# Kernel optimization log

Hardware: AMD Instinct MI355X
Metric: run time of the kernel (lower is better)

## Reference

```python
import jax, jax.numpy as jnp
import numpy as np

DIM_HEAD = 128
HEADS = 16
SCALE = DIM_HEAD ** -0.5


def rotate_half(t):
    # '... (j d) -> ... j d' with j=2: split into first/second halves
    x1, x2 = jnp.split(t, 2, axis=-1)
    return jnp.concatenate((-x2, x1), axis=-1)


def apply_rope(pos, t):
    # pos: [n, d]; t: [..., n, d]
    return t * jnp.cos(pos) + rotate_half(t) * jnp.sin(pos)


def setup_inputs() -> dict:
    key = jax.random.key(0)
    k0, k1, k2, k3 = jax.random.split(key, 4)
    b, n, dim = 2, 2048, 2048
    inner = HEADS * DIM_HEAD
    return {
        "x": jax.random.normal(k0, (b, n, dim), jnp.float32),
        "Wq": jax.random.normal(k1, (dim, inner), jnp.float32) * 0.02,
        "Wkv": jax.random.normal(k2, (dim, 2 * DIM_HEAD), jnp.float32) * 0.02,
        "Wout": jax.random.normal(k3, (inner, dim), jnp.float32) * 0.02,
    }


def reference(x, Wq, Wkv, Wout):
    b, n, dim = x.shape
    # projections from the UN-normalized x (norm in original is dead code)
    q = x @ Wq                               # [b, n, h*d]
    kv = x @ Wkv                             # [b, n, 2d]
    k, v = jnp.split(kv, 2, axis=-1)         # each [b, n, d] (multi-query)
    q = q.reshape(b, n, HEADS, DIM_HEAD).transpose(0, 2, 1, 3)  # [b,h,n,d]

    # rotary positions
    inv_freq = 1.0 / (10000.0 ** (jnp.arange(0, DIM_HEAD, 2, dtype=jnp.float32) / DIM_HEAD))
    freqs = jnp.arange(n, dtype=jnp.float32)[:, None] * inv_freq[None, :]
    pos = jnp.concatenate((freqs, freqs), axis=-1)  # [n, d]

    q = apply_rope(pos, q) * SCALE
    k = apply_rope(pos, k)

    sim = jnp.einsum('bhid,bjd->bhij', q, k)  # [b,h,n,n]
    causal_mask = jnp.triu(jnp.ones((n, n), dtype=bool), 1)
    neg = -jnp.finfo(sim.dtype).max
    sim = jnp.where(causal_mask, neg, sim)
    sim = sim - jax.lax.stop_gradient(jnp.max(sim, axis=-1, keepdims=True))
    attn = jax.nn.softmax(sim, axis=-1)

    out = jnp.einsum('bhij,bjd->bhid', attn, v)          # [b,h,n,d]
    out = out.transpose(0, 2, 1, 3).reshape(b, n, HEADS * DIM_HEAD)
    return out @ Wout
```

## Files before the change

kernel.cpp:

```cpp
#include <hip/hip_runtime.h>
#include <hip/hip_bf16.h>
#include <cstddef>
#include <cstdint>

#define BATCH 2
#define SEQ   2048
#define DIM   2048
#define HEADS 16
#define DHEAD 128
#define INNER (HEADS * DHEAD)
#define MROWS (BATCH * SEQ)
#define ATT_SCALE 0.08838834764831845f
#define QK_SCALE (0.08838834764831845f * 1.4426950408889634f)
#define NEG_LOG2_10000_DIV64 (-13.287712379549449f / 64.0f)
#define M_HAT 12.0f

typedef __attribute__((ext_vector_type(8))) short short8;
typedef __attribute__((ext_vector_type(4))) short short4v;
typedef __attribute__((ext_vector_type(4))) float f32x4;

static __device__ __forceinline__ short f2bf(float x) {
    uint32_t u = __float_as_uint(x);
    uint32_t r = (u + 0x7fffu + ((u >> 16) & 1u)) >> 16;
    return (short)r;
}
static __device__ __forceinline__ float bf2f(short s) {
    return __uint_as_float(((uint32_t)(uint16_t)s) << 16);
}
static __device__ __forceinline__ short2 f2bf2(float a, float b) {
    __hip_bfloat162 h = __float22bfloat162_rn(make_float2(a, b));
    return *reinterpret_cast<short2*>(&h);
}

static __device__ __forceinline__ void glds16(const short* g, short* l) {
    __builtin_amdgcn_global_load_lds(
        (const __attribute__((address_space(1))) unsigned int*)g,
        (__attribute__((address_space(3))) unsigned int*)l, 16, 0, 0);
}

static __device__ __forceinline__ int swz_row(int r) {
    return (r & 3) | ((r >> 1) & 4);
}

static __device__ __forceinline__ void tcast_body(const float* __restrict__ W,
                                                  short* __restrict__ Wt,
                                                  int R, int C, int bx, int by,
                                                  int tid, float (*tile)[65]) {
    const int c0 = bx * 64, r0 = by * 64;
#pragma unroll
    for (int t = 0; t < 4; ++t) {
        int idx = tid + t * 256;
        int row = idx >> 4, col4 = idx & 15;
        float4 v = *(const float4*)&W[(size_t)(r0 + row) * C + c0 + col4 * 4];
        tile[row][col4 * 4 + 0] = v.x;
        tile[row][col4 * 4 + 1] = v.y;
        tile[row][col4 * 4 + 2] = v.z;
        tile[row][col4 * 4 + 3] = v.w;
    }
    __syncthreads();
#pragma unroll
    for (int t = 0; t < 4; ++t) {
        int idx = tid + t * 256;
        int r = idx >> 4, c4 = idx & 15;
        short2 s01 = f2bf2(tile[c4 * 4 + 0][r], tile[c4 * 4 + 1][r]);
        short2 s23 = f2bf2(tile[c4 * 4 + 2][r], tile[c4 * 4 + 3][r]);
        short4v s = {s01.x, s01.y, s23.x, s23.y};
        *(short4v*)&Wt[(size_t)(c0 + r) * R + r0 + c4 * 4] = s;
    }
}

__global__ __launch_bounds__(256) void prep(const float* __restrict__ x,
                                            short* __restrict__ xb,
                                            const float* __restrict__ Wq,
                                            short* __restrict__ Wt,
                                            const float* __restrict__ Wkv,
                                            short* __restrict__ Wkvt,
                                            const float* __restrict__ Wout,
                                            short* __restrict__ WtO,
                                            float2* __restrict__ lut) {
    __shared__ float tile[64][65];
    const int bid = blockIdx.x;
    const int tid = threadIdx.x;
    if (bid < 8192) {
        int i = bid * 256 + tid;
        float4 v = ((const float4*)x)[i];
        short2 s01 = f2bf2(v.x, v.y), s23 = f2bf2(v.z, v.w);
        short4v s = {s01.x, s01.y, s23.x, s23.y};
        ((short4v*)xb)[i] = s;
    } else if (bid < 9216) {
        int t = bid - 8192;
        tcast_body(Wq, Wt, DIM, INNER, t & 31, t >> 5, tid, tile);
    } else if (bid < 9344) {
        int t = bid - 9216;
        tcast_body(Wkv, Wkvt, DIM, 256, t & 3, t >> 2, tid, tile);
    } else if (bid < 10368) {
        int t = bid - 9344;
        tcast_body(Wout, WtO, INNER, DIM, t & 31, t >> 5, tid, tile);
    } else {
        int t = (bid - 10368) * 256 + tid;
        int j = t >> 11;
        int pos = t & (SEQ - 1);
        float ang = (float)pos * exp2f((float)j * NEG_LOG2_10000_DIV64);
        lut[(size_t)j * SEQ + pos] = make_float2(cosf(ang), sinf(ang));
    }
}

__global__ __launch_bounds__(256) void gemm_qkv(const short* __restrict__ A,
                                                const short* __restrict__ Bt,
                                                short* __restrict__ qout,
                                                short* __restrict__ kbout,
                                                short* __restrict__ vtout,
                                                const float2* __restrict__ lut) {
    __shared__ __align__(16) short sA[2][128 * 64];
    __shared__ __align__(16) short sB[2][128 * 64];
    const int K = DIM;

    const int tid = threadIdx.x;
    const int w = tid >> 6, lane = tid & 63;
    const int ln = lane & 15, qr = lane >> 4;
    const int bm = blockIdx.y * 128, bn = blockIdx.x * 128;
    const int wm = (w >> 1) * 64;
    const int wn2 = (w & 1) * 32;

    const f32x4 zero4 = {0.f, 0.f, 0.f, 0.f};
    f32x4 acc[4][4];
#pragma unroll
    for (int mt = 0; mt < 4; ++mt)
#pragma unroll
        for (int nt = 0; nt < 4; ++nt) acc[mt][nt] = zero4;

    int offG[4], ldsO[4];
#pragma unroll
    for (int t = 0; t < 4; ++t) {
        int row = w * 32 + t * 8 + (lane >> 3);
        int c = (lane & 7) ^ (row & 7);
        offG[t] = row * K + c * 8;
        ldsO[t] = (w * 32 + t * 8) * 64;
    }
    const short* pA = A + (size_t)bm * K;
    const short* pB = Bt + (size_t)bn * K;

#pragma unroll
    for (int t = 0; t < 4; ++t) glds16(pA + offG[t], &sA[0][ldsO[t]]);
#pragma unroll
    for (int t = 0; t < 4; ++t) glds16(pB + offG[t], &sB[0][ldsO[t]]);
    __syncthreads();

    const int NT = K / 64;
    for (int kt = 0; kt < NT; ++kt) {
        const int cur = kt & 1;
        if (kt + 1 < NT) {
            const int ko = (kt + 1) * 64;
#pragma unroll
            for (int t = 0; t < 4; ++t)
                glds16(pA + ko + offG[t], &sA[cur ^ 1][ldsO[t]]);
#pragma unroll
            for (int t = 0; t < 4; ++t)
                glds16(pB + ko + offG[t], &sB[cur ^ 1][ldsO[t]]);
        }
#pragma unroll
        for (int ks = 0; ks < 2; ++ks) {
            short8 af[4], bfr[4];
#pragma unroll
            for (int mt = 0; mt < 4; ++mt) {
                const int row = wm + mt * 16 + ln;
                af[mt] = *(const short8*)&sA[cur][row * 64 +
                    (((ks << 2) + qr) ^ (row & 7)) * 8];
            }
#pragma unroll
            for (int nt = 0; nt < 4; ++nt) {
                const int colr = wn2 + ((nt & 1) << 4) + ((nt >> 1) << 6) + ln;
                bfr[nt] = *(const short8*)&sB[cur][colr * 64 +
                    (((ks << 2) + qr) ^ (colr & 7)) * 8];
            }
            __builtin_amdgcn_s_setprio(1);
#pragma unroll
            for (int mt = 0; mt < 4; ++mt)
#pragma unroll
                for (int nt = 0; nt < 4; ++nt)
                    acc[mt][nt] = __builtin_amdgcn_mfma_f32_16x16x32_bf16(
                        af[mt], bfr[nt], acc[mt][nt], 0, 0, 0);
            __builtin_amdgcn_s_setprio(0);
        }
        __syncthreads();
    }

    if (bn <= INNER) {
        const float scale = (bn < INNER) ? QK_SCALE : 1.0f;
#pragma unroll
        for (int mt = 0; mt < 2; ++mt) {  }
#pragma unroll
        for (int mt = 0; mt < 4; ++mt) {
#pragma unroll
            for (int nt = 0; nt < 2; ++nt) {
                const int d0 = wn2 + nt * 16 + ln;
                const int row0 = wm + mt * 16 + qr * 4;
                const int pos0 = (bm + row0) & (SEQ - 1);
                const float4* lp = (const float4*)&lut[(size_t)d0 * SEQ + pos0];
                const float4 c01 = lp[0];
                const float4 c23 = lp[1];
                const float cx[4] = {c01.x, c01.z, c23.x, c23.z};
                const float cy[4] = {c01.y, c01.w, c23.y, c23.w};
#pragma unroll
                for (int r = 0; r < 4; ++r) {
                    const float a = acc[mt][nt][r];
                    const float b = acc[mt][nt + 2][r];
                    const float lo = (a * cx[r] - b * cy[r]) * scale;
                    const float hi = (b * cx[r] + a * cy[r]) * scale;
                    const int row = row0 + r;
                    if (bn < INNER) {
                        short* q0 = qout + (size_t)(bm + row) * INNER + bn + d0;
                        q0[0] = f2bf(lo);
                        q0[64] = f2bf(hi);
                    } else {
                        short* k0p = kbout + (size_t)(bm + row) * DHEAD + d0;
                        k0p[0] = f2bf(lo);
                        k0p[64] = f2bf(hi);
                    }
                }
            }
        }
    } else {
        const int gb = bm >> 11;
        const int pos_base = bm & (SEQ - 1);
#pragma unroll
        for (int mt = 0; mt < 4; ++mt) {
#pragma unroll
            for (int nt = 0; nt < 4; ++nt) {
                const int cn = wn2 + ((nt & 1) << 4) + ((nt >> 1) << 6) + ln;
                const int pos0 = pos_base + wm + mt * 16 + qr * 4;
                short2 s01 = f2bf2(acc[mt][nt][0], acc[mt][nt][1]);
                short2 s23 = f2bf2(acc[mt][nt][2], acc[mt][nt][3]);
                short4v sv = {s01.x, s01.y, s23.x, s23.y};
                *(short4v*)&vtout[((size_t)gb * DHEAD + cn) * SEQ + pos0] = sv;
            }
        }
    }
}

__global__ __launch_bounds__(256) void gemm_bt(const short* __restrict__ A,
                                               const short* __restrict__ Bt,
                                               float* __restrict__ C,
                                               int M, int N, int K) {
    __shared__ __align__(16) short sA[2][128 * 64];
    __shared__ __align__(16) short sB[2][128 * 64];

    const int tid = threadIdx.x;
    const int w = tid >> 6, lane = tid & 63;
    const int ln = lane & 15, qr = lane >> 4;
    const int bm = blockIdx.y * 128, bn = blockIdx.x * 128;
    const int wm = (w >> 1) * 64, wn = (w & 1) * 64;

    const f32x4 zero4 = {0.f, 0.f, 0.f, 0.f};
    f32x4 acc[4][4];
#pragma unroll
    for (int mt = 0; mt < 4; ++mt)
#pragma unroll
        for (int nt = 0; nt < 4; ++nt) acc[mt][nt] = zero4;

    int offG[4], ldsO[4];
#pragma unroll
    for (int t = 0; t < 4; ++t) {
        int row = w * 32 + t * 8 + (lane >> 3);
        int c = (lane & 7) ^ (row & 7);
        offG[t] = row * K + c * 8;
        ldsO[t] = (w * 32 + t * 8) * 64;
    }
    const short* pA = A + (size_t)bm * K;
    const short* pB = Bt + (size_t)bn * K;

#pragma unroll
    for (int t = 0; t < 4; ++t) glds16(pA + offG[t], &sA[0][ldsO[t]]);
#pragma unroll
    for (int t = 0; t < 4; ++t) glds16(pB + offG[t], &sB[0][ldsO[t]]);
    __syncthreads();

    const int NT = 2048 / 64;
    for (int kt = 0; kt < NT; ++kt) {
        const int cur = kt & 1;
        if (kt + 1 < NT) {
            const int ko = (kt + 1) * 64;
#pragma unroll
            for (int t = 0; t < 4; ++t)
                glds16(pA + ko + offG[t], &sA[cur ^ 1][ldsO[t]]);
#pragma unroll
            for (int t = 0; t < 4; ++t)
                glds16(pB + ko + offG[t], &sB[cur ^ 1][ldsO[t]]);
        }
#pragma unroll
        for (int ks = 0; ks < 2; ++ks) {
            short8 af[4], bfr[4];
#pragma unroll
            for (int mt = 0; mt < 4; ++mt) {
                const int row = wm + mt * 16 + ln;
                af[mt] = *(const short8*)&sA[cur][row * 64 +
                    (((ks << 2) + qr) ^ (row & 7)) * 8];
            }
#pragma unroll
            for (int nt = 0; nt < 4; ++nt) {
                const int colr = wn + nt * 16 + ln;
                bfr[nt] = *(const short8*)&sB[cur][colr * 64 +
                    (((ks << 2) + qr) ^ (colr & 7)) * 8];
            }
            __builtin_amdgcn_s_setprio(1);
#pragma unroll
            for (int mt = 0; mt < 4; ++mt)
#pragma unroll
                for (int nt = 0; nt < 4; ++nt)
                    acc[mt][nt] = __builtin_amdgcn_mfma_f32_16x16x32_bf16(
                        af[mt], bfr[nt], acc[mt][nt], 0, 0, 0);
            __builtin_amdgcn_s_setprio(0);
        }
        __syncthreads();
    }

#pragma unroll
    for (int mt = 0; mt < 4; ++mt)
#pragma unroll
        for (int nt = 0; nt < 4; ++nt)
#pragma unroll
            for (int r = 0; r < 4; ++r)
                C[(size_t)(bm + wm + mt * 16 + qr * 4 + r) * N +
                  bn + wn + nt * 16 + ln] = acc[mt][nt][r];
}

__global__ __launch_bounds__(512) void attn_mfma(const short* __restrict__ qb,
                                                 const short* __restrict__ kb,
                                                 const short* __restrict__ vt,
                                                 short* __restrict__ o) {
    __shared__ __align__(16) short sK[2][2][64 * 128];
    __shared__ __align__(16) short sV[2][2][128 * 64];
    __shared__ float lred[4][2][64];

    const int bid = blockIdx.x;
    const int p = bid & 7;
    const int bh = bid >> 3;
    const int h = bh & (HEADS - 1);
    const int b = bh >> 4;

    const int tid = threadIdx.x;
    const int w = tid >> 6;
    const int g = w >> 2;
    const int wg = w & 3;
    const int lane = tid & 63;
    const int ln = lane & 15;
    const int qr = lane >> 4;

    const short* kbase = kb + (size_t)b * SEQ * DHEAD;
    const short* vbase = vt + (size_t)b * DHEAD * SEQ;

    int offK[4], offV[4], ldsK[4], ldsV[4];
#pragma unroll
    for (int t = 0; t < 4; ++t) {
        int rk = wg * 16 + t * 4 + (lane >> 4);
        int ck = (lane & 15) ^ swz_row(rk);
        offK[t] = rk * DHEAD + ck * 8;
        ldsK[t] = (wg * 16 + t * 4) * 128;
        int rv = wg * 32 + t * 8 + (lane >> 3);
        int cv = (lane & 7) ^ swz_row(rv);
        offV[t] = rv * SEQ + cv * 8;
        ldsV[t] = (wg * 32 + t * 8) * 64;
    }

    for (int ph = 0; ph < 2; ++ph) {
        const int it = ph ? p : (15 - p);
        const int i0 = it * 128;
        const int njt = 2 * it + 2;
        const int half = njt >> 1;
        const int igmax = i0 + wg * 32 + 31;

        short8 qf[2][4];
#pragma unroll
        for (int qs = 0; qs < 2; ++qs) {
            const size_t qrow =
                ((size_t)(b * SEQ + i0 + wg * 32 + qs * 16 + ln)) * INNER + h * DHEAD;
#pragma unroll
            for (int ks = 0; ks < 4; ++ks)
                qf[qs][ks] = *(const short8*)&qb[qrow + ks * 32 + qr * 8];
        }

        const f32x4 zero4 = {0.f, 0.f, 0.f, 0.f};
        const f32x4 mhat4 = {-M_HAT, -M_HAT, -M_HAT, -M_HAT};
        f32x4 oa[2][8];
#pragma unroll
        for (int qs = 0; qs < 2; ++qs)
#pragma unroll
            for (int dt = 0; dt < 8; ++dt) oa[qs][dt] = zero4;
        float lsum[2] = {0.f, 0.f};

        __syncthreads();
        {
            const size_t kof = (size_t)g * 64 * DHEAD;
            const size_t vof = (size_t)g * 64;
#pragma unroll
            for (int t = 0; t < 4; ++t)
                glds16(kbase + kof + offK[t], &sK[g][0][ldsK[t]]);
#pragma unroll
            for (int t = 0; t < 4; ++t)
                glds16(vbase + vof + offV[t], &sV[g][0][ldsV[t]]);
        }

        for (int k = 0; k < half; ++k) {
            const int cur = k & 1;
            const int jt = 2 * k + g;
            __syncthreads();
            if (k + 1 < half) {
                const size_t kof = (size_t)(jt + 2) * 64 * DHEAD;
                const size_t vof = (size_t)(jt + 2) * 64;
#pragma unroll
                for (int t = 0; t < 4; ++t)
                    glds16(kbase + kof + offK[t], &sK[g][cur ^ 1][ldsK[t]]);
#pragma unroll
                for (int t = 0; t < 4; ++t)
                    glds16(vbase + vof + offV[t], &sV[g][cur ^ 1][ldsV[t]]);
            }
            if (jt * 64 > igmax) continue;

            f32x4 sacc[2][4];
#pragma unroll
            for (int qs = 0; qs < 2; ++qs)
#pragma unroll
                for (int nt = 0; nt < 4; ++nt) sacc[qs][nt] = mhat4;
            __builtin_amdgcn_s_setprio(1);
#pragma unroll
            for (int nt = 0; nt < 4; ++nt) {
                const int row = ((nt >> 1) << 5) + ((ln >> 2) << 3) +
                                ((nt & 1) << 2) + (ln & 3);
                const int sw = ln & 7;
#pragma unroll
                for (int ks = 0; ks < 4; ++ks) {
                    short8 kf = *(const short8*)&sK[g][cur][row * 128 + ((4 * ks + qr) ^ sw) * 8];
                    sacc[0][nt] = __builtin_amdgcn_mfma_f32_16x16x32_bf16(
                        kf, qf[0][ks], sacc[0][nt], 0, 0, 0);
                    sacc[1][nt] = __builtin_amdgcn_mfma_f32_16x16x32_bf16(
                        kf, qf[1][ks], sacc[1][nt], 0, 0, 0);
                }
            }
            __builtin_amdgcn_s_setprio(0);

            short8 pb[2][2];
#pragma unroll
            for (int qs = 0; qs < 2; ++qs) {
                const int ig = i0 + wg * 32 + qs * 16 + ln;
                if (jt * 64 + 63 > ig) {
#pragma unroll
                    for (int nt = 0; nt < 4; ++nt)
#pragma unroll
                        for (int r = 0; r < 4; ++r) {
                            int jg = jt * 64 + ((nt >> 1) << 5) + qr * 8 +
                                     ((nt & 1) << 2) + r;
                            if (jg > ig) sacc[qs][nt][r] = -3.0e38f;
                        }
                }
                float rs = 0.f;
                float pv[4][4];
#pragma unroll
                for (int nt = 0; nt < 4; ++nt)
#pragma unroll
                    for (int r = 0; r < 4; ++r) {
                        float e = exp2f(sacc[qs][nt][r]);
                        pv[nt][r] = e;
                        rs += e;
                    }
                rs += __shfl_xor(rs, 16);
                rs += __shfl_xor(rs, 32);
                lsum[qs] += rs;
#pragma unroll
                for (int kb2 = 0; kb2 < 2; ++kb2) {
                    short2* pp = (short2*)&pb[qs][kb2];
                    pp[0] = f2bf2(pv[2 * kb2][0], pv[2 * kb2][1]);
                    pp[1] = f2bf2(pv[2 * kb2][2], pv[2 * kb2][3]);
                    pp[2] = f2bf2(pv[2 * kb2 + 1][0], pv[2 * kb2 + 1][1]);
                    pp[3] = f2bf2(pv[2 * kb2 + 1][2], pv[2 * kb2 + 1][3]);
                }
            }

            __builtin_amdgcn_s_setprio(1);
#pragma unroll
            for (int kb2 = 0; kb2 < 2; ++kb2) {
#pragma unroll
                for (int dt = 0; dt < 8; ++dt) {
                    const int row = dt * 16 + ln;
                    short8 vf = *(const short8*)&sV[g][cur][row * 64 +
                        ((4 * kb2 + qr) ^ swz_row(row)) * 8];
                    oa[0][dt] = __builtin_amdgcn_mfma_f32_16x16x32_bf16(
                        vf, pb[0][kb2], oa[0][dt], 0, 0, 0);
                    oa[1][dt] = __builtin_amdgcn_mfma_f32_16x16x32_bf16(
                        vf, pb[1][kb2], oa[1][dt], 0, 0, 0);
                }
            }
            __builtin_amdgcn_s_setprio(0);
        }

        f32x4* cb = (f32x4*)&sK[1][0][0];
        __syncthreads();
        if (g == 1) {
#pragma unroll
            for (int dt = 0; dt < 8; ++dt)
                cb[dt * 256 + wg * 64 + lane] = oa[0][dt];
            lred[wg][0][lane] = lsum[0];
            lred[wg][1][lane] = lsum[1];
        }
        __syncthreads();
        if (g == 0) {
#pragma unroll
            for (int dt = 0; dt < 8; ++dt)
                oa[0][dt] += cb[dt * 256 + wg * 64 + lane];
            lsum[0] += lred[wg][0][lane];
            lsum[1] += lred[wg][1][lane];
        }
        __syncthreads();
        if (g == 1) {
#pragma unroll
            for (int dt = 0; dt < 8; ++dt)
                cb[dt * 256 + wg * 64 + lane] = oa[1][dt];
        }
        __syncthreads();
        if (g == 0) {
#pragma unroll
            for (int dt = 0; dt < 8; ++dt)
                oa[1][dt] += cb[dt * 256 + wg * 64 + lane];
#pragma unroll
            for (int qs = 0; qs < 2; ++qs) {
                const float invl = 1.f / lsum[qs];
                short* orow = o + ((size_t)(b * SEQ + i0 + wg * 32 + qs * 16 + ln)) * INNER +
                              h * DHEAD;
#pragma unroll
                for (int dt = 0; dt < 8; ++dt) {
                    short2 s01 = f2bf2(oa[qs][dt][0] * invl, oa[qs][dt][1] * invl);
                    short2 s23 = f2bf2(oa[qs][dt][2] * invl, oa[qs][dt][3] * invl);
                    short4v sv = {s01.x, s01.y, s23.x, s23.y};
                    *(short4v*)&orow[dt * 16 + qr * 4] = sv;
                }
            }
        }
    }
}

extern "C" void kernel_launch(void* const* d_in, const int* in_sizes, int n_in,
                              void* d_out, int out_size, void* d_ws, size_t ws_size,
                              hipStream_t stream) {
    const float* x    = (const float*)d_in[0];
    const float* Wq   = (const float*)d_in[1];
    const float* Wkv  = (const float*)d_in[2];
    const float* Wout = (const float*)d_in[3];
    float* out = (float*)d_out;

    short* xb    = (short*)d_ws;
    short* Wt    = xb + (size_t)MROWS * DIM;
    short* Wkvt  = Wt + (size_t)DIM * INNER;
    short* WtO   = Wkvt + (size_t)256 * DIM;
    short* qb    = WtO + (size_t)DIM * INNER;
    short* kb    = qb + (size_t)MROWS * INNER;
    short* vt    = kb + (size_t)MROWS * DHEAD;
    float2* lut  = (float2*)(vt + (size_t)BATCH * DHEAD * SEQ);
    short* ob    = xb;

    prep<<<10880, 256, 0, stream>>>(x, xb, Wq, Wt, Wkv, Wkvt, Wout, WtO, lut);
    gemm_qkv<<<dim3(18, 32), 256, 0, stream>>>(xb, Wt, qb, kb, vt, lut);
    attn_mfma<<<256, 512, 0, stream>>>(qb, kb, vt, ob);
    gemm_bt<<<dim3(16, 32), 256, 0, stream>>>(ob, WtO, out, MROWS, DIM, INNER);
}
```

Before: 291.4 us.

## Prefetch two K-tiles ahead in GEMMs using vmcnt waits instead of syncthreads

Both bf16 GEMM kernels (QKV projection and output projection) now issue global-to-LDS loads for tiles kt and kt+1 up front. Inside the loop they wait with s_waitcnt vmcnt(8) so only the current tile must land, rather than draining every outstanding load at __syncthreads. This keeps one tile of loads in flight across each barrier to hide global memory latency. It relies on a hand-coded count of outstanding vector memory ops, which could break if the compiler adds or reorders memory instructions.

Result: faster. 285.3 us (-2.1%).

```diff
diff --git a/kernel.cpp b/kernel.cpp
--- a/kernel.cpp
+++ b/kernel.cpp
@@ -105,6 +105,13 @@
     }
 }
 
+static __device__ __forceinline__ void wait_vmcnt8() {
+    asm volatile("s_waitcnt vmcnt(8)" ::: "memory");
+}
+static __device__ __forceinline__ void wait_vmcnt0() {
+    asm volatile("s_waitcnt vmcnt(0)" ::: "memory");
+}
+
 __global__ __launch_bounds__(256) void gemm_qkv(const short* __restrict__ A,
                                                 const short* __restrict__ Bt,
                                                 short* __restrict__ qout,
@@ -144,20 +151,18 @@
     for (int t = 0; t < 4; ++t) glds16(pA + offG[t], &sA[0][ldsO[t]]);
 #pragma unroll
     for (int t = 0; t < 4; ++t) glds16(pB + offG[t], &sB[0][ldsO[t]]);
-    __syncthreads();
+#pragma unroll
+    for (int t = 0; t < 4; ++t) glds16(pA + 64 + offG[t], &sA[1][ldsO[t]]);
+#pragma unroll
+    for (int t = 0; t < 4; ++t) glds16(pB + 64 + offG[t], &sB[1][ldsO[t]]);
 
     const int NT = K / 64;
     for (int kt = 0; kt < NT; ++kt) {
         const int cur = kt & 1;
-        if (kt + 1 < NT) {
-            const int ko = (kt + 1) * 64;
-#pragma unroll
-            for (int t = 0; t < 4; ++t)
-                glds16(pA + ko + offG[t], &sA[cur ^ 1][ldsO[t]]);
-#pragma unroll
-            for (int t = 0; t < 4; ++t)
-                glds16(pB + ko + offG[t], &sB[cur ^ 1][ldsO[t]]);
-        }
+        if (kt < NT - 2) wait_vmcnt8();
+        else             wait_vmcnt0();
+        __builtin_amdgcn_s_barrier();
+
 #pragma unroll
         for (int ks = 0; ks < 2; ++ks) {
             short8 af[4], bfr[4];
@@ -182,13 +187,21 @@
                         af[mt], bfr[nt], acc[mt][nt], 0, 0, 0);
             __builtin_amdgcn_s_setprio(0);
         }
-        __syncthreads();
+
+        __builtin_amdgcn_s_barrier();
+        if (kt + 2 < NT) {
+            const int ko = (kt + 2) * 64;
+#pragma unroll
+            for (int t = 0; t < 4; ++t)
+                glds16(pA + ko + offG[t], &sA[cur][ldsO[t]]);
+#pragma unroll
+            for (int t = 0; t < 4; ++t)
+                glds16(pB + ko + offG[t], &sB[cur][ldsO[t]]);
+        }
     }
 
     if (bn <= INNER) {
         const float scale = (bn < INNER) ? QK_SCALE : 1.0f;
-#pragma unroll
-        for (int mt = 0; mt < 2; ++mt) {  }
 #pragma unroll
         for (int mt = 0; mt < 4; ++mt) {
 #pragma unroll
@@ -273,20 +286,18 @@
     for (int t = 0; t < 4; ++t) glds16(pA + offG[t], &sA[0][ldsO[t]]);
 #pragma unroll
     for (int t = 0; t < 4; ++t) glds16(pB + offG[t], &sB[0][ldsO[t]]);
-    __syncthreads();
-
-    const int NT = 2048 / 64;
+#pragma unroll
+    for (int t = 0; t < 4; ++t) glds16(pA + 64 + offG[t], &sA[1][ldsO[t]]);
+#pragma unroll
+    for (int t = 0; t < 4; ++t) glds16(pB + 64 + offG[t], &sB[1][ldsO[t]]);
+
+    const int NT = K / 64;
     for (int kt = 0; kt < NT; ++kt) {
         const int cur = kt & 1;
-        if (kt + 1 < NT) {
-            const int ko = (kt + 1) * 64;
-#pragma unroll
-            for (int t = 0; t < 4; ++t)
-                glds16(pA + ko + offG[t], &sA[cur ^ 1][ldsO[t]]);
-#pragma unroll
-            for (int t = 0; t < 4; ++t)
-                glds16(pB + ko + offG[t], &sB[cur ^ 1][ldsO[t]]);
-        }
+        if (kt < NT - 2) wait_vmcnt8();
+        else             wait_vmcnt0();
+        __builtin_amdgcn_s_barrier();
+
 #pragma unroll
         for (int ks = 0; ks < 2; ++ks) {
             short8 af[4], bfr[4];
@@ -311,7 +322,17 @@
                         af[mt], bfr[nt], acc[mt][nt], 0, 0, 0);
             __builtin_amdgcn_s_setprio(0);
         }
-        __syncthreads();
+
+        __builtin_amdgcn_s_barrier();
+        if (kt + 2 < NT) {
+            const int ko = (kt + 2) * 64;
+#pragma unroll
+            for (int t = 0; t < 4; ++t)
+                glds16(pA + ko + offG[t], &sA[cur][ldsO[t]]);
+#pragma unroll
+            for (int t = 0; t < 4; ++t)
+                glds16(pB + ko + offG[t], &sB[cur][ldsO[t]]);
+        }
     }
 
 #pragma unroll
```
